# Optimization experiments

Hardware: AMD Instinct MI355X
Metric: run time of the kernel (lower is better)

The kernel has to match this reference:

```python
import jax, jax.numpy as jnp
import numpy as np

N_E = 16384
E_DIM = 256


def setup_inputs() -> dict:
    key = jax.random.key(0)
    k1, k2 = jax.random.split(key)
    z = jax.random.normal(k1, (16, E_DIM, 32, 32), dtype=jnp.float32)
    # nn.Embedding init: uniform(-1/n_e, 1/n_e)
    embedding_weight = jax.random.uniform(
        k2, (N_E, E_DIM), dtype=jnp.float32, minval=-1.0 / N_E, maxval=1.0 / N_E
    )
    return {"z": z, "embedding_weight": embedding_weight}


def reference(z, embedding_weight):
    # b c h w -> b h w c, flatten to (N, e_dim)
    zf = jnp.transpose(z, (0, 2, 3, 1)).reshape(-1, E_DIM)  # [N, d]
    # squared euclidean distances: ||z||^2 + ||e||^2 - 2 z.e^T
    d = (
        jnp.sum(zf ** 2, axis=1, keepdims=True)          # [N, 1]
        + jnp.sum(embedding_weight ** 2, axis=1)         # [n_e]
        - 2.0 * jnp.einsum("bd,nd->bn", zf, embedding_weight)  # [N, n_e]
    )
    min_encoding_indices = jnp.argmin(d, axis=1)  # [N] int
    return min_encoding_indices
```

## Files before the change

kernel.cpp:

```cpp
#include <hip/hip_runtime.h>

#define EDIM 256
#define NROW 16384
#define NCODE 16384
#define NBN 128
#define MARGIN 2.0e-4f

typedef _Float16 f16x8 __attribute__((ext_vector_type(8)));
typedef _Float16 f16x4 __attribute__((ext_vector_type(4)));
typedef float f32x4 __attribute__((ext_vector_type(4)));

__device__ __forceinline__ void gll16(const void* g, void* l) {
  __builtin_amdgcn_global_load_lds((const __attribute__((address_space(1))) void*)g,
                                   (__attribute__((address_space(3))) void*)l, 16, 0, 0);
}
__device__ __forceinline__ void gll4(const void* g, void* l) {
  __builtin_amdgcn_global_load_lds((const __attribute__((address_space(1))) void*)g,
                                   (__attribute__((address_space(3))) void*)l, 4, 0, 0);
}

__global__ __launch_bounds__(256) void k_prep_e(const float* __restrict__ e,
                                                float* __restrict__ es,
                                                _Float16* __restrict__ Eh) {
  const int row = blockIdx.x * 4 + (threadIdx.x >> 6);
  const int lane = threadIdx.x & 63;
  float4 v = *(const float4*)&e[row * EDIM + lane * 4];
  f16x4 h;
  h[0] = (_Float16)(v.x * 1024.0f);
  h[1] = (_Float16)(v.y * 1024.0f);
  h[2] = (_Float16)(v.z * 1024.0f);
  h[3] = (_Float16)(v.w * 1024.0f);
  *(f16x4*)&Eh[row * EDIM + lane * 4] = h;
  double s = (double)v.x * v.x + (double)v.y * v.y + (double)v.z * v.z + (double)v.w * v.w;
#pragma unroll
  for (int off = 32; off > 0; off >>= 1) s += __shfl_down(s, off, 64);
  if (lane == 0) es[row] = (float)s;
}

__global__ __launch_bounds__(256) void k_es(const float* __restrict__ e,
                                            float* __restrict__ es) {
  const int row = blockIdx.x * 4 + (threadIdx.x >> 6);
  const int lane = threadIdx.x & 63;
  float4 v = *(const float4*)&e[row * EDIM + lane * 4];
  double s = (double)v.x * v.x + (double)v.y * v.y + (double)v.z * v.z + (double)v.w * v.w;
#pragma unroll
  for (int off = 32; off > 0; off >>= 1) s += __shfl_down(s, off, 64);
  if (lane == 0) es[row] = (float)s;
}

__global__ __launch_bounds__(256) void k_cvt_z(const float* __restrict__ z,
                                               _Float16* __restrict__ Zh) {
  __shared__ float zl[EDIM * 64];
  const int t = threadIdx.x;
  const int rb = blockIdx.x;
  const int bb = rb >> 4;
  const int hw0 = (rb & 15) << 6;
  const float* zbase = z + (size_t)bb * EDIM * 1024 + hw0;
#pragma unroll 4
  for (int rep = 0; rep < 64; ++rep) {
    int c = rep * 4 + (t >> 6);
    zl[c * 64 + (t & 63)] = zbase[(size_t)c * 1024 + (t & 63)];
  }
  __syncthreads();
  const int mloc = t >> 2, part = t & 3;
#pragma unroll
  for (int i = 0; i < 8; ++i) {
    int c0 = part * 64 + i * 8;
    f16x8 v;
#pragma unroll
    for (int j = 0; j < 8; ++j) v[j] = (_Float16)zl[(c0 + j) * 64 + mloc];
    *(f16x8*)&Zh[(size_t)(rb * 64 + mloc) * EDIM + c0] = v;
  }
}

__global__ __launch_bounds__(256, 2) void k_gemm(const _Float16* __restrict__ Zh,
                                                 const _Float16* __restrict__ Eh,
                                                 float* __restrict__ lmin,
                                                 uint4* __restrict__ masks) {
  __shared__ __align__(16) char smem[32768];
  char* smemA = smem;
  char* smemB = smem + 16384;

  const int tid = threadIdx.x;
  const int lane = tid & 63;
  const int wv = tid >> 6;
  const int wm = wv & 1, wn = wv >> 1;
  const int fr = lane & 15;
  const int fq = lane >> 4;
  const int swz = (fq ^ ((fr >> 1) & 3)) * 16;

  const int bid = (int)blockIdx.x;
  const int wgid = (bid & 7) * 2048 + (bid >> 3);
  const int st = wgid >> 8, wi = wgid & 255;
  const int bm = ((st & 7) << 4) | (wi & 15);
  const int bn = ((st >> 3) << 4) | (wi >> 4);

  const char* zh_b = (const char*)Zh;
  const char* eh_b = (const char*)Eh;

  auto stage = [&](int buf, int s) {
#pragma unroll
    for (int i = 0; i < 2; ++i) {
      const int L = (i * 256 + tid) * 16;
      const int row = L >> 6, p = (L >> 4) & 3;
      const int gsw = (p ^ ((row >> 1) & 3)) * 16;
      gll16(zh_b + (size_t)(bm * 128 + row) * 512 + s * 64 + gsw, smemA + buf * 8192 + L);
      gll16(eh_b + (size_t)(bn * 128 + row) * 512 + s * 64 + gsw, smemB + buf * 8192 + L);
    }
  };

  f32x4 acc[4][4];
#pragma unroll
  for (int i = 0; i < 4; ++i)
#pragma unroll
    for (int j = 0; j < 4; ++j) acc[i][j] = (f32x4)0.0f;

  stage(0, 0);
  __syncthreads();
#pragma unroll 1
  for (int s = 0; s < 8; ++s) {
    if (s + 1 < 8) stage((s + 1) & 1, s + 1);
    const char* aB = smemA + (s & 1) * 8192;
    const char* bB = smemB + (s & 1) * 8192;
    f16x8 af[4], bf[4];
#pragma unroll
    for (int mi = 0; mi < 4; ++mi)
      af[mi] = *(const f16x8*)(aB + (wm * 64 + mi * 16 + fr) * 64 + swz);
#pragma unroll
    for (int ni = 0; ni < 4; ++ni)
      bf[ni] = *(const f16x8*)(bB + (wn * 64 + ni * 16 + fr) * 64 + swz);
#pragma unroll
    for (int mi = 0; mi < 4; ++mi)
#pragma unroll
      for (int ni = 0; ni < 4; ++ni)
        acc[mi][ni] = __builtin_amdgcn_mfma_f32_16x16x32_f16(af[mi], bf[ni], acc[mi][ni], 0, 0, 0);
    __syncthreads();
  }

  float* rowsmin = (float*)smem;
  float* rowminC = (float*)(smem + 1024);
  unsigned short* msk16 = (unsigned short*)(smem + 1536);
  const float sc = -0.001953125f;
#pragma unroll
  for (int mi = 0; mi < 4; ++mi)
#pragma unroll
    for (int r = 0; r < 4; ++r) {
      float v = acc[mi][0][r] * sc;
      v = fminf(v, acc[mi][1][r] * sc);
      v = fminf(v, acc[mi][2][r] * sc);
      v = fminf(v, acc[mi][3][r] * sc);
#pragma unroll
      for (int off = 1; off < 16; off <<= 1) v = fminf(v, __shfl_xor(v, off, 64));
      if (fr == 0) rowsmin[(wm * 64 + mi * 16 + fq * 4 + r) * 2 + wn] = v;
    }
  __syncthreads();
  if (tid < 128) {
    float rm = fminf(rowsmin[tid * 2], rowsmin[tid * 2 + 1]);
    rowminC[tid] = rm;
    lmin[(size_t)bn * NROW + bm * 128 + tid] = rm;
  }
  __syncthreads();
#pragma unroll
  for (int mi = 0; mi < 4; ++mi)
#pragma unroll
    for (int r = 0; r < 4; ++r) {
      const int row = wm * 64 + mi * 16 + fq * 4 + r;
      const float thr = rowminC[row] + MARGIN;
#pragma unroll
      for (int ni = 0; ni < 4; ++ni) {
        unsigned long long bal = __ballot(acc[mi][ni][r] * sc <= thr);
        if (fr == 0) msk16[row * 8 + wn * 4 + ni] = (unsigned short)((bal >> (fq * 16)) & 0xffffull);
      }
    }
  __syncthreads();
  if (tid < 128)
    masks[(size_t)bn * NROW + bm * 128 + tid] = *(const uint4*)&msk16[tid * 8];
}

__global__ __launch_bounds__(256) void k_rescore(const float* __restrict__ z,
                                                 const float* __restrict__ e,
                                                 const float* __restrict__ es,
                                                 const float* __restrict__ lmin,
                                                 const uint4* __restrict__ masks,
                                                 int* __restrict__ out) {
  extern __shared__ float zl[];
  float* lmin_s = zl + EDIM * 64;
  const int t = threadIdx.x;
  const int rb = (int)blockIdx.x;
  const int bb = rb >> 4;
  const int hw0 = (rb & 15) << 6;
  const int r0 = rb * 64;
  const float* zbase = z + (size_t)bb * EDIM * 1024 + hw0;
#pragma unroll 4
  for (int rep = 0; rep < 64; ++rep) {
    int c = rep * 4 + (t >> 6);
    zl[c * 64 + (t & 63)] = zbase[(size_t)c * 1024 + (t & 63)];
  }
#pragma unroll 4
  for (int i = 0; i < 32; ++i) {
    int bn = i * 4 + (t >> 6);
    lmin_s[bn * 64 + (t & 63)] = lmin[(size_t)bn * NROW + r0 + (t & 63)];
  }
  __syncthreads();

  const int r = t >> 2, q = t & 3;
  const int row = r0 + r;

  double sq = 0.0;
  {
    const float* zq = zl + (q * 64) * 64 + r;
    for (int k = 0; k < 64; ++k) {
      float v = zq[k * 64];
      sq = fma((double)v, (double)v, sq);
    }
  }
  double s01 = sq + __shfl_xor(sq, 1, 64);
  double zsd = s01 + __shfl_xor(s01, 2, 64);
  const float zs = (float)zsd;

  float g = 3.402823466e+38f;
#pragma unroll 8
  for (int j = 0; j < 32; ++j) g = fminf(g, lmin_s[(q * 32 + j) * 64 + r]);
  g = fminf(g, __shfl_xor(g, 1, 64));
  g = fminf(g, __shfl_xor(g, 2, 64));
  const float thr = g + MARGIN;

  float bestd = 3.402823466e+38f;
  int besti = 0x7fffffff;
#pragma unroll 1
  for (int j = 0; j < 32; ++j) {
    const int bn = q * 32 + j;
    if (lmin_s[bn * 64 + r] <= thr) {
      uint4 mk = masks[(size_t)bn * NROW + row];
      unsigned w[4] = {mk.x, mk.y, mk.z, mk.w};
#pragma unroll 1
      for (int qq = 0; qq < 4; ++qq) {
        unsigned u = w[qq];
        while (u) {
          int b = __ffs(u) - 1;
          u &= u - 1;
          const int code = bn * 128 + qq * 32 + b;
          const float* ep = e + (size_t)code * EDIM;
          float dot = 0.0f;
          for (int k = 0; k < EDIM; k += 4) {
            float4 ev = *(const float4*)(ep + k);
            dot = fmaf(zl[(k + 0) * 64 + r], ev.x, dot);
            dot = fmaf(zl[(k + 1) * 64 + r], ev.y, dot);
            dot = fmaf(zl[(k + 2) * 64 + r], ev.z, dot);
            dot = fmaf(zl[(k + 3) * 64 + r], ev.w, dot);
          }
          float d = (zs + es[code]) - 2.0f * dot;
          if (d < bestd) {
            bestd = d;
            besti = code;
          }
        }
      }
    }
  }
#pragma unroll
  for (int off = 1; off <= 2; off <<= 1) {
    float ov = __shfl_xor(bestd, off, 64);
    int oi = __shfl_xor(besti, off, 64);
    if (ov < bestd || (ov == bestd && oi < besti)) {
      bestd = ov;
      besti = oi;
    }
  }
  if (q == 0) out[row] = besti;
}

__global__ __launch_bounds__(256) void k_merge(const float* __restrict__ candv,
                                               const int* __restrict__ candi,
                                               int* __restrict__ out) {
  int n = blockIdx.x * 256 + threadIdx.x;
  float v0 = candv[n], v1 = candv[NROW + n];
  int i0 = candi[n], i1 = candi[NROW + n];
  out[n] = (v1 < v0) ? i1 : i0;
}

template <int SPLIT>
__global__ __launch_bounds__(256, 2) void k_main_fb(const float* __restrict__ z,
                                                    const float* __restrict__ e,
                                                    const float* __restrict__ es,
                                                    float* __restrict__ candv,
                                                    int* __restrict__ candi,
                                                    int* __restrict__ outd) {
  extern __shared__ char smemc[];
  float* As = (float*)smemc;
  float* Bs = (float*)(smemc + 16384);
  double* zred = (double*)(smemc + 16384 + 32768);
  float* zsf = (float*)(smemc + 16384 + 32768 + 2048);
  const int tid = threadIdx.x;
  const int lane = tid & 63;
  const int wv = tid >> 6;
  const int tm = tid & 7;
  const int tn = tid >> 3;
  const int rt = (int)blockIdx.x / SPLIT;
  const int sp = (int)blockIdx.x % SPLIT;
  const int bb = rt >> 4;
  const int hw0 = (rt & 15) << 6;
  const float* zb = z + bb * (EDIM * 1024) + hw0;
  const int codeBase = sp * (NCODE / SPLIT);
  const int NSTEP = (NCODE / SPLIT) / 256 * 8;
  auto stageA = [&](int buf, int gts) {
    const int k0 = (gts & 7) * 32;
    const float* g0 = zb + (size_t)k0 * 1024 + lane;
    float* l0 = As + buf * 2048 + (wv * 8) * 64;
#pragma unroll
    for (int s = 0; s < 8; ++s) gll4(g0 + (size_t)(wv * 8 + s) * 1024, l0 + s * 64);
  };
  float4 bpre[8];
  auto loadB = [&](int gts) {
    const int ct = gts >> 3, k0 = (gts & 7) * 32;
    const float* g = e + (size_t)(codeBase + ct * 256 + tid) * 256 + k0;
#pragma unroll
    for (int s = 0; s < 8; ++s) bpre[s] = *(const float4*)(g + s * 4);
  };
  auto writeB = [&](int buf) {
    float* bw_ = Bs + buf * 8192 + tid;
#pragma unroll
    for (int s = 0; s < 8; ++s) {
      bw_[(4 * s + 0) * 256] = bpre[s].x;
      bw_[(4 * s + 1) * 256] = bpre[s].y;
      bw_[(4 * s + 2) * 256] = bpre[s].z;
      bw_[(4 * s + 3) * 256] = bpre[s].w;
    }
  };
  stageA(0, 0);
  loadB(0);
  {
    const int m = tid & 63, qt = tid >> 6;
    const float* zp = zb + (size_t)(qt * 64) * 1024 + m;
    double s = 0.0;
    for (int k = 0; k < 64; ++k) {
      float v = zp[(size_t)k * 1024];
      s = fma((double)v, (double)v, s);
    }
    zred[qt * 64 + m] = s;
  }
  writeB(0);
  __syncthreads();
  if (tid < 64) {
    double sz = (zred[tid] + zred[64 + tid]) + (zred[128 + tid] + zred[192 + tid]);
    zsf[tid] = (float)sz;
  }
  __syncthreads();
  float zsr[8];
#pragma unroll
  for (int i = 0; i < 8; ++i) zsr[i] = zsf[tm * 8 + i];
  __syncthreads();
  float bestv[8];
  int besti[8];
#pragma unroll
  for (int i = 0; i < 8; ++i) {
    bestv[i] = 3.402823466e+38f;
    besti[i] = 0;
  }
  float acc[8][8];
  int cur = 0;
#pragma unroll 1
  for (int step = 0; step < NSTEP; ++step) {
    const int kc = step & 7, ct = step >> 3;
    if (step + 1 < NSTEP) {
      stageA(cur ^ 1, step + 1);
      loadB(step + 1);
    }
    if (kc == 0) {
#pragma unroll
      for (int i = 0; i < 8; ++i)
#pragma unroll
        for (int j = 0; j < 8; ++j) acc[i][j] = 0.0f;
    }
    const float* ak = As + cur * 2048 + tm * 8;
    const float* bk = Bs + cur * 8192 + tn * 8;
#pragma unroll 4
    for (int k = 0; k < 32; ++k) {
      float4 a0 = *(const float4*)(ak + k * 64);
      float4 a1 = *(const float4*)(ak + k * 64 + 4);
      float4 b0 = *(const float4*)(bk + k * 256);
      float4 b1 = *(const float4*)(bk + k * 256 + 4);
      float av[8] = {a0.x, a0.y, a0.z, a0.w, a1.x, a1.y, a1.z, a1.w};
      float bw[8] = {b0.x, b0.y, b0.z, b0.w, b1.x, b1.y, b1.z, b1.w};
#pragma unroll
      for (int i = 0; i < 8; ++i)
#pragma unroll
        for (int j = 0; j < 8; ++j) acc[i][j] = fmaf(av[i], bw[j], acc[i][j]);
    }
    if (step + 1 < NSTEP) writeB(cur ^ 1);
    if (kc == 7) {
      const int cb = codeBase + ct * 256 + tn * 8;
#pragma unroll
      for (int j = 0; j < 8; ++j) {
        float ej = es[cb + j];
#pragma unroll
        for (int i = 0; i < 8; ++i) {
          float d = (zsr[i] + ej) - 2.0f * acc[i][j];
          if (d < bestv[i]) {
            bestv[i] = d;
            besti[i] = cb + j;
          }
        }
      }
    }
    __syncthreads();
    cur ^= 1;
  }
  float* Lv = (float*)(smemc + 16384);
  int* Li = (int*)(smemc + 16384 + 8192);
#pragma unroll
  for (int i = 0; i < 8; ++i) {
    Lv[(tm * 8 + i) * 32 + tn] = bestv[i];
    Li[(tm * 8 + i) * 32 + tn] = besti[i];
  }
  __syncthreads();
  if (tid < 64) {
    float bv = Lv[tid * 32];
    int bi = Li[tid * 32];
#pragma unroll 1
    for (int g2 = 1; g2 < 32; ++g2) {
      float v = Lv[tid * 32 + g2];
      int ii = Li[tid * 32 + g2];
      if (v < bv || (v == bv && ii < bi)) {
        bv = v;
        bi = ii;
      }
    }
    if (SPLIT == 1) outd[rt * 64 + tid] = bi;
    else {
      candv[sp * NROW + rt * 64 + tid] = bv;
      candi[sp * NROW + rt * 64 + tid] = bi;
    }
  }
}

extern "C" void kernel_launch(void* const* d_in, const int* in_sizes, int n_in,
                              void* d_out, int out_size, void* d_ws, size_t ws_size,
                              hipStream_t stream) {
  const float* z = (const float*)d_in[0];
  const float* e = (const float*)d_in[1];
  int* out = (int*)d_out;

  char* ws = (char*)d_ws;
  float* es = (float*)ws;
  const size_t off_zh = 65536;
  const size_t off_eh = off_zh + (size_t)NROW * EDIM * 2;
  const size_t off_lmin = off_eh + (size_t)NCODE * EDIM * 2;
  const size_t off_masks = off_lmin + (size_t)NROW * NBN * 4;
  const size_t need = off_masks + (size_t)NROW * NBN * 16;

  if (ws_size >= need) {
    _Float16* Zh = (_Float16*)(ws + off_zh);
    _Float16* Eh = (_Float16*)(ws + off_eh);
    float* lmin = (float*)(ws + off_lmin);
    uint4* masks = (uint4*)(ws + off_masks);
    k_prep_e<<<dim3(NCODE / 4), dim3(256), 0, stream>>>(e, es, Eh);
    k_cvt_z<<<dim3(256), dim3(256), 0, stream>>>(z, Zh);
    k_gemm<<<dim3(16384), dim3(256), 0, stream>>>(Zh, Eh, lmin, masks);
    hipFuncSetAttribute(reinterpret_cast<const void*>(&k_rescore),
                        hipFuncAttributeMaxDynamicSharedMemorySize, 98304);
    k_rescore<<<dim3(256), dim3(256), 98304, stream>>>(z, e, es, lmin, masks, out);
  } else {
    k_es<<<dim3(NCODE / 4), dim3(256), 0, stream>>>(e, es);
    float* candv = (float*)(ws + 65536);
    int* candi = (int*)(ws + 65536 + 131072);
    const size_t smem = 16384 + 65536;
    if (ws_size >= 65536 + 131072 + 131072) {
      hipFuncSetAttribute(reinterpret_cast<const void*>(&k_main_fb<2>),
                          hipFuncAttributeMaxDynamicSharedMemorySize, (int)smem);
      k_main_fb<2><<<dim3(512), dim3(256), smem, stream>>>(z, e, es, candv, candi, out);
      k_merge<<<dim3(NROW / 256), dim3(256), 0, stream>>>(candv, candi, out);
    } else {
      hipFuncSetAttribute(reinterpret_cast<const void*>(&k_main_fb<1>),
                          hipFuncAttributeMaxDynamicSharedMemorySize, (int)smem);
      k_main_fb<1><<<dim3(256), dim3(256), smem, stream>>>(z, e, es, candv, candi, out);
    }
  }
}
```

Before: 407.7 us.

## Load codebook fragments directly from global in GEMM and halve rescore row blocks

The GEMM kernel stops staging the E tile through LDS. Each wave now reads its B fragments straight from global memory, while only the Z tile is staged, with a wider 128-byte K step and an XOR swizzle. Launch bounds drop the occupancy hint of 2. The conversion and rescore kernels now process 32 rows per block instead of 64, using padded LDS (stride 33) and twice the blocks, which lowers shared memory per block and raises parallelism. Direct global B loads depend on L1/L2 reuse and may add latency to the inner loop.

```diff
diff --git a/kernel.cpp b/kernel.cpp
--- a/kernel.cpp
+++ b/kernel.cpp
@@ -50,36 +50,34 @@
 
 __global__ __launch_bounds__(256) void k_cvt_z(const float* __restrict__ z,
                                                _Float16* __restrict__ Zh) {
-  __shared__ float zl[EDIM * 64];
+  __shared__ float zl[EDIM * 33];
   const int t = threadIdx.x;
   const int rb = blockIdx.x;
-  const int bb = rb >> 4;
-  const int hw0 = (rb & 15) << 6;
+  const int bb = rb >> 5;
+  const int hw0 = (rb & 31) << 5;
   const float* zbase = z + (size_t)bb * EDIM * 1024 + hw0;
 #pragma unroll 4
-  for (int rep = 0; rep < 64; ++rep) {
-    int c = rep * 4 + (t >> 6);
-    zl[c * 64 + (t & 63)] = zbase[(size_t)c * 1024 + (t & 63)];
-  }
-  __syncthreads();
-  const int mloc = t >> 2, part = t & 3;
-#pragma unroll
-  for (int i = 0; i < 8; ++i) {
-    int c0 = part * 64 + i * 8;
+  for (int rep = 0; rep < 32; ++rep) {
+    int c = rep * 8 + (t >> 5);
+    zl[c * 33 + (t & 31)] = zbase[(size_t)c * 1024 + (t & 31)];
+  }
+  __syncthreads();
+  const int mloc = t >> 3, part = t & 7;
+#pragma unroll
+  for (int i = 0; i < 4; ++i) {
+    int c0 = part * 32 + i * 8;
     f16x8 v;
 #pragma unroll
-    for (int j = 0; j < 8; ++j) v[j] = (_Float16)zl[(c0 + j) * 64 + mloc];
-    *(f16x8*)&Zh[(size_t)(rb * 64 + mloc) * EDIM + c0] = v;
-  }
-}
-
-__global__ __launch_bounds__(256, 2) void k_gemm(const _Float16* __restrict__ Zh,
-                                                 const _Float16* __restrict__ Eh,
-                                                 float* __restrict__ lmin,
-                                                 uint4* __restrict__ masks) {
+    for (int j = 0; j < 8; ++j) v[j] = (_Float16)zl[(c0 + j) * 33 + mloc];
+    *(f16x8*)&Zh[(size_t)(rb * 32 + mloc) * EDIM + c0] = v;
+  }
+}
+
+__global__ __launch_bounds__(256) void k_gemm(const _Float16* __restrict__ Zh,
+                                              const _Float16* __restrict__ Eh,
+                                              float* __restrict__ lmin,
+                                              uint4* __restrict__ masks) {
   __shared__ __align__(16) char smem[32768];
-  char* smemA = smem;
-  char* smemB = smem + 16384;
 
   const int tid = threadIdx.x;
   const int lane = tid & 63;
@@ -87,7 +85,6 @@
   const int wm = wv & 1, wn = wv >> 1;
   const int fr = lane & 15;
   const int fq = lane >> 4;
-  const int swz = (fq ^ ((fr >> 1) & 3)) * 16;
 
   const int bid = (int)blockIdx.x;
   const int wgid = (bid & 7) * 2048 + (bid >> 3);
@@ -97,15 +94,15 @@
 
   const char* zh_b = (const char*)Zh;
   const char* eh_b = (const char*)Eh;
+  const char* ebase = eh_b + (size_t)(bn * 128 + wn * 64 + fr) * 512 + fq * 16;
 
   auto stage = [&](int buf, int s) {
 #pragma unroll
-    for (int i = 0; i < 2; ++i) {
+    for (int i = 0; i < 4; ++i) {
       const int L = (i * 256 + tid) * 16;
-      const int row = L >> 6, p = (L >> 4) & 3;
-      const int gsw = (p ^ ((row >> 1) & 3)) * 16;
-      gll16(zh_b + (size_t)(bm * 128 + row) * 512 + s * 64 + gsw, smemA + buf * 8192 + L);
-      gll16(eh_b + (size_t)(bn * 128 + row) * 512 + s * 64 + gsw, smemB + buf * 8192 + L);
+      const int row = L >> 7, p = (L >> 4) & 7;
+      gll16(zh_b + (size_t)(bm * 128 + row) * 512 + s * 128 + ((p ^ (row & 7)) * 16),
+            smem + buf * 16384 + L);
     }
   };
 
@@ -117,24 +114,41 @@
 
   stage(0, 0);
   __syncthreads();
+  int buf = 0;
 #pragma unroll 1
-  for (int s = 0; s < 8; ++s) {
-    if (s + 1 < 8) stage((s + 1) & 1, s + 1);
-    const char* aB = smemA + (s & 1) * 8192;
-    const char* bB = smemB + (s & 1) * 8192;
-    f16x8 af[4], bf[4];
-#pragma unroll
-    for (int mi = 0; mi < 4; ++mi)
-      af[mi] = *(const f16x8*)(aB + (wm * 64 + mi * 16 + fr) * 64 + swz);
-#pragma unroll
-    for (int ni = 0; ni < 4; ++ni)
-      bf[ni] = *(const f16x8*)(bB + (wn * 64 + ni * 16 + fr) * 64 + swz);
-#pragma unroll
-    for (int mi = 0; mi < 4; ++mi)
+  for (int s = 0; s < 4; ++s) {
+    if (s + 1 < 4) stage(buf ^ 1, s + 1);
+    const char* aB = smem + buf * 16384;
+    {
+      f16x8 bf[4], af[4];
 #pragma unroll
       for (int ni = 0; ni < 4; ++ni)
-        acc[mi][ni] = __builtin_amdgcn_mfma_f32_16x16x32_f16(af[mi], bf[ni], acc[mi][ni], 0, 0, 0);
+        bf[ni] = *(const f16x8*)(ebase + (size_t)(ni * 16) * 512 + s * 128);
+#pragma unroll
+      for (int mi = 0; mi < 4; ++mi)
+        af[mi] = *(const f16x8*)(aB + (wm * 64 + mi * 16 + fr) * 128 + ((fq ^ (fr & 7)) * 16));
+#pragma unroll
+      for (int mi = 0; mi < 4; ++mi)
+#pragma unroll
+        for (int ni = 0; ni < 4; ++ni)
+          acc[mi][ni] = __builtin_amdgcn_mfma_f32_16x16x32_f16(af[mi], bf[ni], acc[mi][ni], 0, 0, 0);
+    }
+    {
+      f16x8 bf[4], af[4];
+#pragma unroll
+      for (int ni = 0; ni < 4; ++ni)
+        bf[ni] = *(const f16x8*)(ebase + (size_t)(ni * 16) * 512 + s * 128 + 64);
+#pragma unroll
+      for (int mi = 0; mi < 4; ++mi)
+        af[mi] = *(const f16x8*)(aB + (wm * 64 + mi * 16 + fr) * 128 + (((4 + fq) ^ (fr & 7)) * 16));
+#pragma unroll
+      for (int mi = 0; mi < 4; ++mi)
+#pragma unroll
+        for (int ni = 0; ni < 4; ++ni)
+          acc[mi][ni] = __builtin_amdgcn_mfma_f32_16x16x32_f16(af[mi], bf[ni], acc[mi][ni], 0, 0, 0);
+    }
     __syncthreads();
+    buf ^= 1;
   }
 
   float* rowsmin = (float*)smem;
@@ -184,33 +198,33 @@
                                                  const uint4* __restrict__ masks,
                                                  int* __restrict__ out) {
   extern __shared__ float zl[];
-  float* lmin_s = zl + EDIM * 64;
+  float* lmin_s = zl + EDIM * 33;
   const int t = threadIdx.x;
   const int rb = (int)blockIdx.x;
-  const int bb = rb >> 4;
-  const int hw0 = (rb & 15) << 6;
-  const int r0 = rb * 64;
+  const int bb = rb >> 5;
+  const int hw0 = (rb & 31) << 5;
+  const int r0 = rb * 32;
   const float* zbase = z + (size_t)bb * EDIM * 1024 + hw0;
 #pragma unroll 4
-  for (int rep = 0; rep < 64; ++rep) {
-    int c = rep * 4 + (t >> 6);
-    zl[c * 64 + (t & 63)] = zbase[(size_t)c * 1024 + (t & 63)];
+  for (int rep = 0; rep < 32; ++rep) {
+    int c = rep * 8 + (t >> 5);
+    zl[c * 33 + (t & 31)] = zbase[(size_t)c * 1024 + (t & 31)];
   }
 #pragma unroll 4
-  for (int i = 0; i < 32; ++i) {
-    int bn = i * 4 + (t >> 6);
-    lmin_s[bn * 64 + (t & 63)] = lmin[(size_t)bn * NROW + r0 + (t & 63)];
-  }
-  __syncthreads();
-
-  const int r = t >> 2, q = t & 3;
+  for (int rep = 0; rep < 16; ++rep) {
+    int bn = rep * 8 + (t >> 5);
+    lmin_s[bn * 33 + (t & 31)] = lmin[(size_t)bn * NROW + r0 + (t & 31)];
+  }
+  __syncthreads();
+
+  const int r = t >> 3, q8 = t & 7, q = q8 & 3;
   const int row = r0 + r;
 
   double sq = 0.0;
   {
-    const float* zq = zl + (q * 64) * 64 + r;
+    const float* zq = zl + (q * 64) * 33 + r;
     for (int k = 0; k < 64; ++k) {
-      float v = zq[k * 64];
+      float v = zq[k * 33];
       sq = fma((double)v, (double)v, sq);
     }
   }
@@ -219,18 +233,19 @@
   const float zs = (float)zsd;
 
   float g = 3.402823466e+38f;
-#pragma unroll 8
-  for (int j = 0; j < 32; ++j) g = fminf(g, lmin_s[(q * 32 + j) * 64 + r]);
+#pragma unroll
+  for (int j = 0; j < 16; ++j) g = fminf(g, lmin_s[(q8 * 16 + j) * 33 + r]);
   g = fminf(g, __shfl_xor(g, 1, 64));
   g = fminf(g, __shfl_xor(g, 2, 64));
+  g = fminf(g, __shfl_xor(g, 4, 64));
   const float thr = g + MARGIN;
 
   float bestd = 3.402823466e+38f;
   int besti = 0x7fffffff;
 #pragma unroll 1
-  for (int j = 0; j < 32; ++j) {
-    const int bn = q * 32 + j;
-    if (lmin_s[bn * 64 + r] <= thr) {
+  for (int j = 0; j < 16; ++j) {
+    const int bn = q8 * 16 + j;
+    if (lmin_s[bn * 33 + r] <= thr) {
       uint4 mk = masks[(size_t)bn * NROW + row];
       unsigned w[4] = {mk.x, mk.y, mk.z, mk.w};
 #pragma unroll 1
@@ -244,10 +259,10 @@
           float dot = 0.0f;
           for (int k = 0; k < EDIM; k += 4) {
             float4 ev = *(const float4*)(ep + k);
-            dot = fmaf(zl[(k + 0) * 64 + r], ev.x, dot);
-            dot = fmaf(zl[(k + 1) * 64 + r], ev.y, dot);
-            dot = fmaf(zl[(k + 2) * 64 + r], ev.z, dot);
-            dot = fmaf(zl[(k + 3) * 64 + r], ev.w, dot);
+            dot = fmaf(zl[(k + 0) * 33 + r], ev.x, dot);
+            dot = fmaf(zl[(k + 1) * 33 + r], ev.y, dot);
+            dot = fmaf(zl[(k + 2) * 33 + r], ev.z, dot);
+            dot = fmaf(zl[(k + 3) * 33 + r], ev.w, dot);
           }
           float d = (zs + es[code]) - 2.0f * dot;
           if (d < bestd) {
@@ -259,7 +274,7 @@
     }
   }
 #pragma unroll
-  for (int off = 1; off <= 2; off <<= 1) {
+  for (int off = 1; off <= 4; off <<= 1) {
     float ov = __shfl_xor(bestd, off, 64);
     int oi = __shfl_xor(besti, off, 64);
     if (ov < bestd || (ov == bestd && oi < besti)) {
@@ -267,7 +282,7 @@
       besti = oi;
     }
   }
-  if (q == 0) out[row] = besti;
+  if (q8 == 0) out[row] = besti;
 }
 
 __global__ __launch_bounds__(256) void k_merge(const float* __restrict__ candv,
@@ -455,11 +470,12 @@
     float* lmin = (float*)(ws + off_lmin);
     uint4* masks = (uint4*)(ws + off_masks);
     k_prep_e<<<dim3(NCODE / 4), dim3(256), 0, stream>>>(e, es, Eh);
-    k_cvt_z<<<dim3(256), dim3(256), 0, stream>>>(z, Zh);
+    k_cvt_z<<<dim3(512), dim3(256), 0, stream>>>(z, Zh);
     k_gemm<<<dim3(16384), dim3(256), 0, stream>>>(Zh, Eh, lmin, masks);
+    const int rs_smem = (EDIM * 33 + NBN * 33) * 4;
     hipFuncSetAttribute(reinterpret_cast<const void*>(&k_rescore),
-                        hipFuncAttributeMaxDynamicSharedMemorySize, 98304);
-    k_rescore<<<dim3(256), dim3(256), 98304, stream>>>(z, e, es, lmin, masks, out);
+                        hipFuncAttributeMaxDynamicSharedMemorySize, rs_smem);
+    k_rescore<<<dim3(512), dim3(256), rs_smem, stream>>>(z, e, es, lmin, masks, out);
   } else {
     k_es<<<dim3(NCODE / 4), dim3(256), 0, stream>>>(e, es);
     float* candv = (float*)(ws + 65536);
```

Measured after the change: 458.9 us. +12.6%, slower.
